# Optimization experiments

Measured on AMD Instinct MI355X. Metric: run time of the kernel, lower is better.

The kernel has to match this reference:

```python
import jax, jax.numpy as jnp
import numpy as np

ROPE_BASE = 10000.0
NUM_HEADS = 16
NUM_KV_HEADS = 4


def _rms_norm(x, eps):
    # F.rms_norm with no weight: x / sqrt(mean(x^2) + eps)
    return x * jax.lax.rsqrt(jnp.mean(x * x, axis=-1, keepdims=True) + eps)


def _apply_rope(x, cos, sin):
    h = x.shape[-1] // 2
    x1, x2 = x[..., :h], x[..., h:]
    return jnp.concatenate([x1 * cos + x2 * sin, -x1 * sin + x2 * cos], axis=-1)


def setup_inputs() -> dict:
    key = jax.random.key(0)
    ks = jax.random.split(key, 5)
    B, T, D = 2, 2048, 1024
    H, Hkv = NUM_HEADS, NUM_KV_HEADS
    hd = D // H
    kv_dim = Hkv * hd
    s_in = 1.0 / np.sqrt(D)
    return {
        "x": jax.random.normal(ks[0], (B, T, D), dtype=jnp.float32),
        "Wq": jax.random.normal(ks[1], (D, D), dtype=jnp.float32) * s_in,
        "Wk": jax.random.normal(ks[2], (kv_dim, D), dtype=jnp.float32) * s_in,
        "Wv": jax.random.normal(ks[3], (kv_dim, D), dtype=jnp.float32) * s_in,
        "Wproj": jax.random.normal(ks[4], (D, D), dtype=jnp.float32) * s_in,
        "q_gain": jnp.full((H,), 1.0, dtype=jnp.float32),
    }


def reference(x, Wq, Wk, Wv, Wproj, q_gain):
    B, T, D = x.shape
    H, Hkv = NUM_HEADS, NUM_KV_HEADS
    hd = D // H
    rep = H // Hkv
    eps = jnp.finfo(x.dtype).eps

    # QKV projections (F.linear: x @ W.T)
    q = jnp.einsum('btd,od->bto', x, Wq).reshape(B, T, H, hd).transpose(0, 2, 1, 3)
    k = jnp.einsum('btd,od->bto', x, Wk).reshape(B, T, Hkv, hd).transpose(0, 2, 1, 3)
    v = jnp.einsum('btd,od->bto', x, Wv).reshape(B, T, Hkv, hd).transpose(0, 2, 1, 3)

    q = _rms_norm(q, eps)
    k = _rms_norm(k, eps)

    # RoPE tables: [1, 1, T, hd/2]
    inv_freq = 1.0 / (ROPE_BASE ** (jnp.arange(0, hd, 2, dtype=jnp.float32) / hd))
    f = jnp.arange(T, dtype=jnp.float32)[:, None] * inv_freq[None, :]
    cos = jnp.cos(f)[None, None].astype(q.dtype)
    sin = jnp.sin(f)[None, None].astype(q.dtype)
    q = _apply_rope(q, cos, sin)
    k = _apply_rope(k, cos, sin)

    q = q * q_gain.astype(q.dtype)[None, :, None, None]

    # GQA without materializing repeated K/V: group q heads [Hkv, rep]
    qg = q.reshape(B, Hkv, rep, T, hd)
    scale = hd ** -0.5
    scores = jnp.einsum('bgrqd,bgkd->bgrqk', qg, k) * scale
    causal = jnp.tril(jnp.ones((T, T), dtype=bool))
    scores = jnp.where(causal, scores, -jnp.inf)
    att = jax.nn.softmax(scores.astype(jnp.float32), axis=-1).astype(q.dtype)
    y = jnp.einsum('bgrqk,bgkd->bgrqd', att, v)  # [B,Hkv,rep,T,hd]
    y = y.reshape(B, H, T, hd).transpose(0, 2, 1, 3).reshape(B, T, D)
    return jnp.einsum('btd,od->bto', y, Wproj)
```

## Files before the change

kernel.cpp:

```cpp
#include <hip/hip_runtime.h>
#include <cstdint>
#include <cstddef>

typedef __attribute__((ext_vector_type(8))) short short8;
typedef __attribute__((ext_vector_type(4))) float floatx4;
typedef __attribute__((ext_vector_type(4))) short short4v;
typedef unsigned short u16;
typedef unsigned int u32;

#define B_   2
#define T_   2048
#define D_   1024
#define H_   16
#define HKV_ 4
#define HD_  64
#define KV_  256
#define M_   4096
#define QS_  1536

#define NX   4194304
#define NWQ  1048576
#define NWK  262144
#define NWV  262144
#define NWP  1048576
#define NCAST (NX + NWQ + NWK + NWV + NWP)
#define CAST_BLOCKS (NCAST / 1024)
#define TAB_BLOCKS  256

__device__ __forceinline__ float b2f(u16 u) {
    union { u32 i; float f; } v; v.i = ((u32)u) << 16; return v.f;
}
__device__ __forceinline__ u16 f2b(float f) {
    union { float f; u32 i; } v; v.f = f;
    u32 r = v.i + 0x7FFF + ((v.i >> 16) & 1);
    return (u16)(r >> 16);
}
__device__ __forceinline__ u32 pack_hi(float a, float b) {
    union { float f; u32 u; } ua, ub; ua.f = a; ub.f = b;
    return (ua.u >> 16) | (ub.u & 0xFFFF0000u);
}

__device__ __forceinline__ void async16(const u16* g, u16* l) {
    __builtin_amdgcn_global_load_lds(
        (const __attribute__((address_space(1))) u32*)g,
        (__attribute__((address_space(3))) u32*)l, 16, 0, 0);
}

__global__ __launch_bounds__(256) void prep(const float* __restrict__ x,
                                            const float* __restrict__ wq,
                                            const float* __restrict__ wk,
                                            const float* __restrict__ wv,
                                            const float* __restrict__ wp,
                                            u16* __restrict__ dst,
                                            float2* __restrict__ tab) {
    int blk = blockIdx.x;
    if (blk < CAST_BLOCKS) {
        int i = blk * 1024 + threadIdx.x * 4;
        const float* src; int off;
        if      (i < NX)                  { src = x;  off = i; }
        else if (i < NX+NWQ)              { src = wq; off = i - NX; }
        else if (i < NX+NWQ+NWK)          { src = wk; off = i - (NX+NWQ); }
        else if (i < NX+NWQ+NWK+NWV)      { src = wv; off = i - (NX+NWQ+NWK); }
        else                              { src = wp; off = i - (NX+NWQ+NWK+NWV); }
        float4 v = *(const float4*)(src + off);
        short4v o;
        o.x = (short)f2b(v.x); o.y = (short)f2b(v.y);
        o.z = (short)f2b(v.z); o.w = (short)f2b(v.w);
        *(short4v*)(dst + i) = o;
    } else {
        int idx = (blk - CAST_BLOCKS) * 256 + threadIdx.x;
        int t = idx >> 5, i = idx & 31;
        float freq = exp2f(-(float)i * (13.287712379549449f / 32.0f));
        float ang = (float)t * freq;
        tab[idx] = make_float2(cosf(ang), sinf(ang));
    }
}

__global__ __launch_bounds__(256, 3) void gemm_qkv(const u16* __restrict__ A,
                                                   const u16* __restrict__ W,
                                                   u16* __restrict__ C,
                                                   u16* __restrict__ Vt,
                                                   const float* __restrict__ gain,
                                                   const float2* __restrict__ tab) {
    const int K = D_;
    __shared__ u16 As[2][128 * 32];
    __shared__ u16 Bs[2][64 * 32];
    const int t = threadIdx.x;
    const int wave = t >> 6, lane = t & 63;
    const int quad = lane >> 4, l16 = lane & 15;
    const int wm = wave * 32;
    const int m0 = blockIdx.y * 128, n0 = blockIdx.x * 64;

    floatx4 acc[2][4];
#pragma unroll
    for (int i = 0; i < 2; i++)
#pragma unroll
        for (int j = 0; j < 4; j++) acc[i][j] = (floatx4){0.f, 0.f, 0.f, 0.f};

    const int sr = t >> 2, sc = (t & 3) * 8;
    const u16* ga = A + (size_t)(m0 + sr) * K + sc;
    const u16* gb = W + (size_t)(n0 + sr) * K + sc;

    async16(ga, As[0] + t * 8);
    async16(ga + (size_t)64 * K, As[0] + t * 8 + 64 * 32);
    async16(gb, Bs[0] + t * 8);

    int cur = 0;
    for (int kt = 0; kt < K; kt += 32) {
        __syncthreads();
        if (kt + 32 < K) {
            const u16* ga2 = ga + kt + 32;
            const u16* gb2 = gb + kt + 32;
            async16(ga2, As[cur ^ 1] + t * 8);
            async16(ga2 + (size_t)64 * K, As[cur ^ 1] + t * 8 + 64 * 32);
            async16(gb2, Bs[cur ^ 1] + t * 8);
        }
        short8 af[2], bf[4];
#pragma unroll
        for (int mt = 0; mt < 2; mt++)
            af[mt] = *(const short8*)(As[cur] + (wm + mt * 16 + l16) * 32 + quad * 8);
#pragma unroll
        for (int nt = 0; nt < 4; nt++)
            bf[nt] = *(const short8*)(Bs[cur] + (nt * 16 + l16) * 32 + quad * 8);
#pragma unroll
        for (int mt = 0; mt < 2; mt++)
#pragma unroll
            for (int nt = 0; nt < 4; nt++)
                acc[mt][nt] = __builtin_amdgcn_mfma_f32_16x16x32_bf16(
                    af[mt], bf[nt], acc[mt][nt], 0, 0, 0);
        cur ^= 1;
    }

    const int col0 = n0;
    if (col0 < 1280) {
        float gs = (col0 < 1024)
                 ? gain[col0 >> 6] * (0.125f * 1.4426950408889634f)
                 : 1.0f;
#pragma unroll
        for (int mt = 0; mt < 2; mt++)
#pragma unroll
            for (int r = 0; r < 4; r++) {
                int row = m0 + wm + mt * 16 + quad * 4 + r;
                int tt = row & (T_ - 1);
                float v0 = acc[mt][0][r], v1 = acc[mt][1][r];
                float v2 = acc[mt][2][r], v3 = acc[mt][3][r];
                float ss = v0 * v0 + v1 * v1 + v2 * v2 + v3 * v3;
                ss += __shfl_xor(ss, 1); ss += __shfl_xor(ss, 2);
                ss += __shfl_xor(ss, 4); ss += __shfl_xor(ss, 8);
                float inv = rsqrtf(ss * (1.0f / 64.0f) + 1.1920929e-7f);
                v0 *= inv; v1 *= inv; v2 *= inv; v3 *= inv;
                float2 cs0 = tab[tt * 32 + l16];
                float2 cs1 = tab[tt * 32 + 16 + l16];
                float o0 = (v0 * cs0.x + v2 * cs0.y) * gs;
                float o1 = (v1 * cs1.x + v3 * cs1.y) * gs;
                float o2 = (v2 * cs0.x - v0 * cs0.y) * gs;
                float o3 = (v3 * cs1.x - v1 * cs1.y) * gs;
                u16* cp = C + (size_t)row * QS_ + col0 + l16;
                cp[0]  = f2b(o0);
                cp[16] = f2b(o1);
                cp[32] = f2b(o2);
                cp[48] = f2b(o3);
            }
    } else {
        const int g = (col0 - 1280) >> 6;
#pragma unroll
        for (int mt = 0; mt < 2; mt++)
#pragma unroll
            for (int r = 0; r < 4; r++) {
                int row = m0 + wm + mt * 16 + quad * 4 + r;
                int tt = row & (T_ - 1);
                int bb = row >> 11;
#pragma unroll
                for (int nt = 0; nt < 4; nt++)
                    Vt[(size_t)((bb * 4 + g) * 64 + nt * 16 + l16) * T_ + tt] =
                        f2b(acc[mt][nt][r]);
            }
    }
}

__global__ __launch_bounds__(256, 3) void gemm_proj(const u16* __restrict__ A,
                                                    const u16* __restrict__ W,
                                                    float* __restrict__ C) {
    const int K = D_;
    __shared__ u16 As[2][128 * 32];
    __shared__ u16 Bs[2][64 * 32];
    const int t = threadIdx.x;
    const int wave = t >> 6, lane = t & 63;
    const int quad = lane >> 4, l16 = lane & 15;
    const int wm = wave * 32;
    const int m0 = blockIdx.y * 128, n0 = blockIdx.x * 64;

    floatx4 acc[2][4];
#pragma unroll
    for (int i = 0; i < 2; i++)
#pragma unroll
        for (int j = 0; j < 4; j++) acc[i][j] = (floatx4){0.f, 0.f, 0.f, 0.f};

    const int sr = t >> 2, sc = (t & 3) * 8;
    const u16* ga = A + (size_t)(m0 + sr) * K + sc;
    const u16* gb = W + (size_t)(n0 + sr) * K + sc;

    async16(ga, As[0] + t * 8);
    async16(ga + (size_t)64 * K, As[0] + t * 8 + 64 * 32);
    async16(gb, Bs[0] + t * 8);

    int cur = 0;
    for (int kt = 0; kt < K; kt += 32) {
        __syncthreads();
        if (kt + 32 < K) {
            const u16* ga2 = ga + kt + 32;
            const u16* gb2 = gb + kt + 32;
            async16(ga2, As[cur ^ 1] + t * 8);
            async16(ga2 + (size_t)64 * K, As[cur ^ 1] + t * 8 + 64 * 32);
            async16(gb2, Bs[cur ^ 1] + t * 8);
        }
        short8 af[2], bf[4];
#pragma unroll
        for (int mt = 0; mt < 2; mt++)
            af[mt] = *(const short8*)(As[cur] + (wm + mt * 16 + l16) * 32 + quad * 8);
#pragma unroll
        for (int nt = 0; nt < 4; nt++)
            bf[nt] = *(const short8*)(Bs[cur] + (nt * 16 + l16) * 32 + quad * 8);
#pragma unroll
        for (int mt = 0; mt < 2; mt++)
#pragma unroll
            for (int nt = 0; nt < 4; nt++)
                acc[mt][nt] = __builtin_amdgcn_mfma_f32_16x16x32_bf16(
                    af[mt], bf[nt], acc[mt][nt], 0, 0, 0);
        cur ^= 1;
    }

#pragma unroll
    for (int mt = 0; mt < 2; mt++)
#pragma unroll
        for (int nt = 0; nt < 4; nt++)
#pragma unroll
            for (int r = 0; r < 4; r++) {
                int row = m0 + wm + mt * 16 + quad * 4 + r;
                int col = n0 + nt * 16 + l16;
                C[(size_t)row * D_ + col] = acc[mt][nt][r];
            }
}

__global__ __launch_bounds__(256) void flash(const u16* __restrict__ QKV,
                                             const u16* __restrict__ Vtr,
                                             u16* __restrict__ Y) {
    const int xp = blockIdx.x;
    const int h  = blockIdx.y;
    const int b  = blockIdx.z;
    const int g  = h >> 2;
    const int w    = threadIdx.x >> 6;
    const int lane = threadIdx.x & 63;
    const int quad = lane >> 4, l16 = lane & 15;

    __shared__ u16 Kt[64 * 64];
    __shared__ u16 Vs[64 * 64];
    __shared__ __align__(16) u16 P[4][2][16][72];

    const int mA = xp * 64 + w * 16;
    const int mB = (31 - xp) * 64 + w * 16;
    const int nA = xp + 1;
    const int nB = 32 - xp;

    const u16* qpA = QKV + (size_t)(b * T_ + mA + l16) * QS_ + h * HD_ + quad * 8;
    const u16* qpB = QKV + (size_t)(b * T_ + mB + l16) * QS_ + h * HD_ + quad * 8;
    short8 aqA0 = *(const short8*)(qpA);
    short8 aqA1 = *(const short8*)(qpA + 32);
    short8 aqB0 = *(const short8*)(qpB);
    short8 aqB1 = *(const short8*)(qpB + 32);

    short8 ones;
#pragma unroll
    for (int i = 0; i < 8; i++) ones[i] = (short)0x3F80;

    floatx4 accA[4], accB[4];
#pragma unroll
    for (int i = 0; i < 4; i++) {
        accA[i] = (floatx4){0.f, 0.f, 0.f, 0.f};
        accB[i] = (floatx4){0.f, 0.f, 0.f, 0.f};
    }
    floatx4 lAcc = (floatx4){0.f, 0.f, 0.f, 0.f};
    floatx4 lBcc = (floatx4){0.f, 0.f, 0.f, 0.f};

    const int srow = w * 16 + (lane >> 3);
    const int sseg = (lane & 7) ^ ((lane >> 3) & 7);
    const u16* kg = QKV + (size_t)(b * T_ + srow) * QS_ + D_ + g * 64 + sseg * 8;
    const u16* vg = Vtr + (size_t)((b * 4 + g) * 64 + srow) * T_ + sseg * 8;
    u16* klds = Kt + w * 1024 + lane * 8;
    u16* vlds = Vs + w * 1024 + lane * 8;

    const int sw0 = (quad ^ (l16 & 7)) * 8;
    const int sw1 = ((4 + quad) ^ (l16 & 7)) * 8;

    async16(kg, klds);
    async16(kg + (size_t)8 * QS_, klds + 512);
    async16(vg, vlds);
    async16(vg + (size_t)8 * T_, vlds + 512);

    for (int tk = 0; tk < nB; tk++) {
        const bool dual = (tk < nA);
        __syncthreads();

        floatx4 SB[4], SA[4];
#pragma unroll
        for (int nt = 0; nt < 4; nt++) {
            const u16* kr = Kt + (nt * 16 + l16) * 64;
            short8 kf0 = *(const short8*)(kr + sw0);
            short8 kf1 = *(const short8*)(kr + sw1);
            SB[nt] = (floatx4){0.f, 0.f, 0.f, 0.f};
            SB[nt] = __builtin_amdgcn_mfma_f32_16x16x32_bf16(kf0, aqB0, SB[nt], 0, 0, 0);
            SB[nt] = __builtin_amdgcn_mfma_f32_16x16x32_bf16(kf1, aqB1, SB[nt], 0, 0, 0);
            if (dual) {
                SA[nt] = (floatx4){0.f, 0.f, 0.f, 0.f};
                SA[nt] = __builtin_amdgcn_mfma_f32_16x16x32_bf16(kf0, aqA0, SA[nt], 0, 0, 0);
                SA[nt] = __builtin_amdgcn_mfma_f32_16x16x32_bf16(kf1, aqA1, SA[nt], 0, 0, 0);
            }
        }
        short8 vf[4][2];
#pragma unroll
        for (int dd = 0; dd < 4; dd++) {
            const u16* vr = Vs + (dd * 16 + l16) * 64;
            vf[dd][0] = *(const short8*)(vr + sw0);
            vf[dd][1] = *(const short8*)(vr + sw1);
        }
        __syncthreads();
        if (tk + 1 < nB) {
            kg += (size_t)64 * QS_;
            vg += 64;
            async16(kg, klds);
            async16(kg + (size_t)8 * QS_, klds + 512);
            async16(vg, vlds);
            async16(vg + (size_t)8 * T_, vlds + 512);
        }

        const bool maskB = (tk == nB - 1);
        const int qB = mB + l16;
#pragma unroll
        for (int nt = 0; nt < 4; nt++) {
            float p[4];
#pragma unroll
            for (int r = 0; r < 4; r++) {
                float e = __builtin_amdgcn_exp2f(SB[nt][r]);
                if (maskB) {
                    int key = tk * 64 + nt * 16 + quad * 4 + r;
                    e = (key <= qB) ? e : 0.f;
                }
                p[r] = e;
            }
            uint2 pw; pw.x = pack_hi(p[0], p[1]); pw.y = pack_hi(p[2], p[3]);
            *(uint2*)&P[w][1][l16][nt * 16 + quad * 4] = pw;
        }
        short8 pfB0 = *(const short8*)&P[w][1][l16][quad * 8];
        short8 pfB1 = *(const short8*)&P[w][1][l16][quad * 8 + 32];
#pragma unroll
        for (int dd = 0; dd < 4; dd++) {
            accB[dd] = __builtin_amdgcn_mfma_f32_16x16x32_bf16(pfB0, vf[dd][0], accB[dd], 0, 0, 0);
            accB[dd] = __builtin_amdgcn_mfma_f32_16x16x32_bf16(pfB1, vf[dd][1], accB[dd], 0, 0, 0);
        }
        lBcc = __builtin_amdgcn_mfma_f32_16x16x32_bf16(pfB0, ones, lBcc, 0, 0, 0);
        lBcc = __builtin_amdgcn_mfma_f32_16x16x32_bf16(pfB1, ones, lBcc, 0, 0, 0);

        if (dual) {
            const bool maskA = (tk == nA - 1);
            const int qA = mA + l16;
#pragma unroll
            for (int nt = 0; nt < 4; nt++) {
                float p[4];
#pragma unroll
                for (int r = 0; r < 4; r++) {
                    float e = __builtin_amdgcn_exp2f(SA[nt][r]);
                    if (maskA) {
                        int key = tk * 64 + nt * 16 + quad * 4 + r;
                        e = (key <= qA) ? e : 0.f;
                    }
                    p[r] = e;
                }
                uint2 pw; pw.x = pack_hi(p[0], p[1]); pw.y = pack_hi(p[2], p[3]);
                *(uint2*)&P[w][0][l16][nt * 16 + quad * 4] = pw;
            }
            short8 pfA0 = *(const short8*)&P[w][0][l16][quad * 8];
            short8 pfA1 = *(const short8*)&P[w][0][l16][quad * 8 + 32];
#pragma unroll
            for (int dd = 0; dd < 4; dd++) {
                accA[dd] = __builtin_amdgcn_mfma_f32_16x16x32_bf16(pfA0, vf[dd][0], accA[dd], 0, 0, 0);
                accA[dd] = __builtin_amdgcn_mfma_f32_16x16x32_bf16(pfA1, vf[dd][1], accA[dd], 0, 0, 0);
            }
            lAcc = __builtin_amdgcn_mfma_f32_16x16x32_bf16(pfA0, ones, lAcc, 0, 0, 0);
            lAcc = __builtin_amdgcn_mfma_f32_16x16x32_bf16(pfA1, ones, lAcc, 0, 0, 0);
        }
    }

#pragma unroll
    for (int r = 0; r < 4; r++) {
        float invA = 1.0f / lAcc[r];
        float invB = 1.0f / lBcc[r];
        int rowA = mA + quad * 4 + r;
        int rowB = mB + quad * 4 + r;
        u16* ypA = Y + (size_t)(b * T_ + rowA) * D_ + h * HD_ + l16;
        u16* ypB = Y + (size_t)(b * T_ + rowB) * D_ + h * HD_ + l16;
#pragma unroll
        for (int dd = 0; dd < 4; dd++) {
            ypA[dd * 16] = f2b(accA[dd][r] * invA);
            ypB[dd * 16] = f2b(accB[dd][r] * invB);
        }
    }
}

extern "C" void kernel_launch(void* const* d_in, const int* in_sizes, int n_in,
                              void* d_out, int out_size, void* d_ws, size_t ws_size,
                              hipStream_t stream) {
    const float* x    = (const float*)d_in[0];
    const float* Wq   = (const float*)d_in[1];
    const float* Wk   = (const float*)d_in[2];
    const float* Wv   = (const float*)d_in[3];
    const float* Wp   = (const float*)d_in[4];
    const float* gain = (const float*)d_in[5];
    float* out = (float*)d_out;

    u16* xb   = (u16*)d_ws;
    u16* Wcat = xb + (size_t)NX;
    u16* Wpb  = Wcat + (size_t)(NWQ + NWK + NWV);
    u16* QKV  = Wpb + (size_t)NWP;
    u16* Vt   = QKV + (size_t)M_ * QS_;
    u16* Y    = Vt + (size_t)M_ * KV_;
    float2* tab = (float2*)(Y + (size_t)M_ * D_);

    prep<<<CAST_BLOCKS + TAB_BLOCKS, 256, 0, stream>>>(x, Wq, Wk, Wv, Wp, xb, tab);

    gemm_qkv<<<dim3(QS_ / 64, M_ / 128), 256, 0, stream>>>(xb, Wcat, QKV, Vt,
                                                           gain, tab);

    flash<<<dim3(16, H_, B_), 256, 0, stream>>>(QKV, Vt, Y);

    gemm_proj<<<dim3(D_ / 64, M_ / 128), 256, 0, stream>>>(Y, Wpb, out);
}
```

Baseline: 174.1 us.

## Split flash KV range and proj GEMM K across more blocks with atomics

The flash kernel grid doubles: each original pair of query tiles is split so later query rows' key ranges are divided between two blocks. Partial unnormalized outputs and row sums for the second half of the sequence go to fp32 buffers via atomics, and a new combine kernel normalizes them into Y. The projection GEMM is split-K in two with atomicAdd into a zeroed output. The aim is more blocks and better CU occupancy, at the cost of memsets, atomic traffic, an extra kernel launch and non-deterministic summation order.

```diff
diff --git a/kernel.cpp b/kernel.cpp
--- a/kernel.cpp
+++ b/kernel.cpp
@@ -189,6 +189,7 @@
     const int quad = lane >> 4, l16 = lane & 15;
     const int wm = wave * 32;
     const int m0 = blockIdx.y * 128, n0 = blockIdx.x * 64;
+    const int kbase = blockIdx.z * 512;
 
     floatx4 acc[2][4];
 #pragma unroll
@@ -197,17 +198,17 @@
         for (int j = 0; j < 4; j++) acc[i][j] = (floatx4){0.f, 0.f, 0.f, 0.f};
 
     const int sr = t >> 2, sc = (t & 3) * 8;
-    const u16* ga = A + (size_t)(m0 + sr) * K + sc;
-    const u16* gb = W + (size_t)(n0 + sr) * K + sc;
+    const u16* ga = A + (size_t)(m0 + sr) * K + kbase + sc;
+    const u16* gb = W + (size_t)(n0 + sr) * K + kbase + sc;
 
     async16(ga, As[0] + t * 8);
     async16(ga + (size_t)64 * K, As[0] + t * 8 + 64 * 32);
     async16(gb, Bs[0] + t * 8);
 
     int cur = 0;
-    for (int kt = 0; kt < K; kt += 32) {
+    for (int kt = 0; kt < 512; kt += 32) {
         __syncthreads();
-        if (kt + 32 < K) {
+        if (kt + 32 < 512) {
             const u16* ga2 = ga + kt + 32;
             const u16* gb2 = gb + kt + 32;
             async16(ga2, As[cur ^ 1] + t * 8);
@@ -238,14 +239,16 @@
             for (int r = 0; r < 4; r++) {
                 int row = m0 + wm + mt * 16 + quad * 4 + r;
                 int col = n0 + nt * 16 + l16;
-                C[(size_t)row * D_ + col] = acc[mt][nt][r];
-            }
-}
-
-__global__ __launch_bounds__(256) void flash(const u16* __restrict__ QKV,
-                                             const u16* __restrict__ Vtr,
-                                             u16* __restrict__ Y) {
-    const int xp = blockIdx.x;
+                atomicAdd(&C[(size_t)row * D_ + col], acc[mt][nt][r]);
+            }
+}
+
+__global__ __launch_bounds__(256, 4) void flash(const u16* __restrict__ QKV,
+                                                const u16* __restrict__ Vtr,
+                                                u16* __restrict__ Y,
+                                                float* __restrict__ Oacc,
+                                                float* __restrict__ Lacc) {
+    const int u  = blockIdx.x;
     const int h  = blockIdx.y;
     const int b  = blockIdx.z;
     const int g  = h >> 2;
@@ -255,155 +258,148 @@
 
     __shared__ u16 Kt[64 * 64];
     __shared__ u16 Vs[64 * 64];
-    __shared__ __align__(16) u16 P[4][2][16][72];
-
-    const int mA = xp * 64 + w * 16;
-    const int mB = (31 - xp) * 64 + w * 16;
-    const int nA = xp + 1;
-    const int nB = 32 - xp;
-
-    const u16* qpA = QKV + (size_t)(b * T_ + mA + l16) * QS_ + h * HD_ + quad * 8;
-    const u16* qpB = QKV + (size_t)(b * T_ + mB + l16) * QS_ + h * HD_ + quad * 8;
-    short8 aqA0 = *(const short8*)(qpA);
-    short8 aqA1 = *(const short8*)(qpA + 32);
-    short8 aqB0 = *(const short8*)(qpB);
-    short8 aqB1 = *(const short8*)(qpB + 32);
-
-    short8 ones;
-#pragma unroll
-    for (int i = 0; i < 8; i++) ones[i] = (short)0x3F80;
-
-    floatx4 accA[4], accB[4];
-#pragma unroll
-    for (int i = 0; i < 4; i++) {
-        accA[i] = (floatx4){0.f, 0.f, 0.f, 0.f};
-        accB[i] = (floatx4){0.f, 0.f, 0.f, 0.f};
-    }
-    floatx4 lAcc = (floatx4){0.f, 0.f, 0.f, 0.f};
-    floatx4 lBcc = (floatx4){0.f, 0.f, 0.f, 0.f};
+    __shared__ __align__(16) u16 P[4][16][72];
+
+    const int xp = u & 15;
+    const int nseg = (u < 16) ? 2 : 1;
+    int m0s[2], k0s[2], k1s[2];
+    if (u < 16) {
+        m0s[0] = xp * 64;        k0s[0] = 0;  k1s[0] = xp + 1;
+        m0s[1] = (31 - xp) * 64; k0s[1] = 16; k1s[1] = 32 - xp;
+    } else {
+        m0s[0] = (31 - xp) * 64; k0s[0] = 0;  k1s[0] = 16;
+        m0s[1] = 0; k0s[1] = 0; k1s[1] = 0;
+    }
 
     const int srow = w * 16 + (lane >> 3);
     const int sseg = (lane & 7) ^ ((lane >> 3) & 7);
-    const u16* kg = QKV + (size_t)(b * T_ + srow) * QS_ + D_ + g * 64 + sseg * 8;
-    const u16* vg = Vtr + (size_t)((b * 4 + g) * 64 + srow) * T_ + sseg * 8;
+    const u16* kgb = QKV + (size_t)(b * T_ + srow) * QS_ + D_ + g * 64 + sseg * 8;
+    const u16* vgb = Vtr + (size_t)((b * 4 + g) * 64 + srow) * T_ + sseg * 8;
     u16* klds = Kt + w * 1024 + lane * 8;
     u16* vlds = Vs + w * 1024 + lane * 8;
-
     const int sw0 = (quad ^ (l16 & 7)) * 8;
     const int sw1 = ((4 + quad) ^ (l16 & 7)) * 8;
 
-    async16(kg, klds);
-    async16(kg + (size_t)8 * QS_, klds + 512);
-    async16(vg, vlds);
-    async16(vg + (size_t)8 * T_, vlds + 512);
-
-    for (int tk = 0; tk < nB; tk++) {
-        const bool dual = (tk < nA);
-        __syncthreads();
-
-        floatx4 SB[4], SA[4];
-#pragma unroll
-        for (int nt = 0; nt < 4; nt++) {
-            const u16* kr = Kt + (nt * 16 + l16) * 64;
-            short8 kf0 = *(const short8*)(kr + sw0);
-            short8 kf1 = *(const short8*)(kr + sw1);
-            SB[nt] = (floatx4){0.f, 0.f, 0.f, 0.f};
-            SB[nt] = __builtin_amdgcn_mfma_f32_16x16x32_bf16(kf0, aqB0, SB[nt], 0, 0, 0);
-            SB[nt] = __builtin_amdgcn_mfma_f32_16x16x32_bf16(kf1, aqB1, SB[nt], 0, 0, 0);
-            if (dual) {
-                SA[nt] = (floatx4){0.f, 0.f, 0.f, 0.f};
-                SA[nt] = __builtin_amdgcn_mfma_f32_16x16x32_bf16(kf0, aqA0, SA[nt], 0, 0, 0);
-                SA[nt] = __builtin_amdgcn_mfma_f32_16x16x32_bf16(kf1, aqA1, SA[nt], 0, 0, 0);
-            }
-        }
-        short8 vf[4][2];
-#pragma unroll
-        for (int dd = 0; dd < 4; dd++) {
-            const u16* vr = Vs + (dd * 16 + l16) * 64;
-            vf[dd][0] = *(const short8*)(vr + sw0);
-            vf[dd][1] = *(const short8*)(vr + sw1);
-        }
-        __syncthreads();
-        if (tk + 1 < nB) {
-            kg += (size_t)64 * QS_;
-            vg += 64;
-            async16(kg, klds);
-            async16(kg + (size_t)8 * QS_, klds + 512);
-            async16(vg, vlds);
-            async16(vg + (size_t)8 * T_, vlds + 512);
-        }
-
-        const bool maskB = (tk == nB - 1);
-        const int qB = mB + l16;
-#pragma unroll
-        for (int nt = 0; nt < 4; nt++) {
-            float p[4];
-#pragma unroll
-            for (int r = 0; r < 4; r++) {
-                float e = __builtin_amdgcn_exp2f(SB[nt][r]);
-                if (maskB) {
-                    int key = tk * 64 + nt * 16 + quad * 4 + r;
-                    e = (key <= qB) ? e : 0.f;
-                }
-                p[r] = e;
-            }
-            uint2 pw; pw.x = pack_hi(p[0], p[1]); pw.y = pack_hi(p[2], p[3]);
-            *(uint2*)&P[w][1][l16][nt * 16 + quad * 4] = pw;
-        }
-        short8 pfB0 = *(const short8*)&P[w][1][l16][quad * 8];
-        short8 pfB1 = *(const short8*)&P[w][1][l16][quad * 8 + 32];
-#pragma unroll
-        for (int dd = 0; dd < 4; dd++) {
-            accB[dd] = __builtin_amdgcn_mfma_f32_16x16x32_bf16(pfB0, vf[dd][0], accB[dd], 0, 0, 0);
-            accB[dd] = __builtin_amdgcn_mfma_f32_16x16x32_bf16(pfB1, vf[dd][1], accB[dd], 0, 0, 0);
-        }
-        lBcc = __builtin_amdgcn_mfma_f32_16x16x32_bf16(pfB0, ones, lBcc, 0, 0, 0);
-        lBcc = __builtin_amdgcn_mfma_f32_16x16x32_bf16(pfB1, ones, lBcc, 0, 0, 0);
-
-        if (dual) {
-            const bool maskA = (tk == nA - 1);
-            const int qA = mA + l16;
+    auto stage = [&](int tile) {
+        const u16* kg = kgb + (size_t)tile * 64 * QS_;
+        const u16* vg = vgb + (size_t)tile * 64;
+        async16(kg, klds);
+        async16(kg + (size_t)8 * QS_, klds + 512);
+        async16(vg, vlds);
+        async16(vg + (size_t)8 * T_, vlds + 512);
+    };
+
+    short8 ones;
+#pragma unroll
+    for (int i = 0; i < 8; i++) ones[i] = (short)0x3F80;
+
+    stage(k0s[0]);
+
+    for (int seg = 0; seg < nseg; ++seg) {
+        const int mseg = m0s[seg], k0 = k0s[seg], k1 = k1s[seg];
+        const int jt = mseg >> 6;
+        const int m = mseg + w * 16;
+
+        const u16* qp = QKV + (size_t)(b * T_ + m + l16) * QS_ + h * HD_ + quad * 8;
+        short8 aq0 = *(const short8*)(qp);
+        short8 aq1 = *(const short8*)(qp + 32);
+
+        floatx4 acc[4];
+#pragma unroll
+        for (int i = 0; i < 4; i++) acc[i] = (floatx4){0.f, 0.f, 0.f, 0.f};
+        floatx4 lAcc = (floatx4){0.f, 0.f, 0.f, 0.f};
+
+        for (int tk = k0; tk < k1; ++tk) {
+            __syncthreads();
+
+            floatx4 S[4];
+#pragma unroll
+            for (int nt = 0; nt < 4; nt++) {
+                const u16* kr = Kt + (nt * 16 + l16) * 64;
+                short8 kf0 = *(const short8*)(kr + sw0);
+                short8 kf1 = *(const short8*)(kr + sw1);
+                S[nt] = (floatx4){0.f, 0.f, 0.f, 0.f};
+                S[nt] = __builtin_amdgcn_mfma_f32_16x16x32_bf16(kf0, aq0, S[nt], 0, 0, 0);
+                S[nt] = __builtin_amdgcn_mfma_f32_16x16x32_bf16(kf1, aq1, S[nt], 0, 0, 0);
+            }
+            short8 vf[4][2];
+#pragma unroll
+            for (int dd = 0; dd < 4; dd++) {
+                const u16* vr = Vs + (dd * 16 + l16) * 64;
+                vf[dd][0] = *(const short8*)(vr + sw0);
+                vf[dd][1] = *(const short8*)(vr + sw1);
+            }
+            __syncthreads();
+
+            int nxt = (tk + 1 < k1) ? tk + 1 : ((seg + 1 < nseg) ? k0s[seg + 1] : -1);
+            if (nxt >= 0) stage(nxt);
+
+            const bool msk = (tk == jt);
+            const int qq = m + l16;
 #pragma unroll
             for (int nt = 0; nt < 4; nt++) {
                 float p[4];
 #pragma unroll
                 for (int r = 0; r < 4; r++) {
-                    float e = __builtin_amdgcn_exp2f(SA[nt][r]);
-                    if (maskA) {
+                    float e = __builtin_amdgcn_exp2f(S[nt][r]);
+                    if (msk) {
                         int key = tk * 64 + nt * 16 + quad * 4 + r;
-                        e = (key <= qA) ? e : 0.f;
+                        e = (key <= qq) ? e : 0.f;
                     }
                     p[r] = e;
                 }
                 uint2 pw; pw.x = pack_hi(p[0], p[1]); pw.y = pack_hi(p[2], p[3]);
-                *(uint2*)&P[w][0][l16][nt * 16 + quad * 4] = pw;
-            }
-            short8 pfA0 = *(const short8*)&P[w][0][l16][quad * 8];
-            short8 pfA1 = *(const short8*)&P[w][0][l16][quad * 8 + 32];
+                *(uint2*)&P[w][l16][nt * 16 + quad * 4] = pw;
+            }
+            short8 pf0 = *(const short8*)&P[w][l16][quad * 8];
+            short8 pf1 = *(const short8*)&P[w][l16][quad * 8 + 32];
 #pragma unroll
             for (int dd = 0; dd < 4; dd++) {
-                accA[dd] = __builtin_amdgcn_mfma_f32_16x16x32_bf16(pfA0, vf[dd][0], accA[dd], 0, 0, 0);
-                accA[dd] = __builtin_amdgcn_mfma_f32_16x16x32_bf16(pfA1, vf[dd][1], accA[dd], 0, 0, 0);
-            }
-            lAcc = __builtin_amdgcn_mfma_f32_16x16x32_bf16(pfA0, ones, lAcc, 0, 0, 0);
-            lAcc = __builtin_amdgcn_mfma_f32_16x16x32_bf16(pfA1, ones, lAcc, 0, 0, 0);
+                acc[dd] = __builtin_amdgcn_mfma_f32_16x16x32_bf16(pf0, vf[dd][0], acc[dd], 0, 0, 0);
+                acc[dd] = __builtin_amdgcn_mfma_f32_16x16x32_bf16(pf1, vf[dd][1], acc[dd], 0, 0, 0);
+            }
+            lAcc = __builtin_amdgcn_mfma_f32_16x16x32_bf16(pf0, ones, lAcc, 0, 0, 0);
+            lAcc = __builtin_amdgcn_mfma_f32_16x16x32_bf16(pf1, ones, lAcc, 0, 0, 0);
         }
-    }
-
-#pragma unroll
-    for (int r = 0; r < 4; r++) {
-        float invA = 1.0f / lAcc[r];
-        float invB = 1.0f / lBcc[r];
-        int rowA = mA + quad * 4 + r;
-        int rowB = mB + quad * 4 + r;
-        u16* ypA = Y + (size_t)(b * T_ + rowA) * D_ + h * HD_ + l16;
-        u16* ypB = Y + (size_t)(b * T_ + rowB) * D_ + h * HD_ + l16;
-#pragma unroll
-        for (int dd = 0; dd < 4; dd++) {
-            ypA[dd * 16] = f2b(accA[dd][r] * invA);
-            ypB[dd * 16] = f2b(accB[dd][r] * invB);
+
+        if (u < 16 && seg == 0) {
+#pragma unroll
+            for (int r = 0; r < 4; r++) {
+                float inv = 1.0f / lAcc[r];
+                int row = m + quad * 4 + r;
+                u16* yp = Y + (size_t)(b * T_ + row) * D_ + h * HD_ + l16;
+#pragma unroll
+                for (int dd = 0; dd < 4; dd++)
+                    yp[dd * 16] = f2b(acc[dd][r] * inv);
+            }
+        } else {
+#pragma unroll
+            for (int r = 0; r < 4; r++) {
+                int rp = m + quad * 4 + r - 1024;
+                float* op = Oacc + (size_t)(b * 1024 + rp) * 1024 + h * HD_ + l16;
+#pragma unroll
+                for (int dd = 0; dd < 4; dd++)
+                    atomicAdd(op + dd * 16, acc[dd][r]);
+                if (l16 == 0)
+                    atomicAdd(Lacc + (b * 1024 + rp) * 16 + h, lAcc[r]);
+            }
         }
     }
+}
+
+__global__ __launch_bounds__(256) void combine(const float* __restrict__ Oacc,
+                                               const float* __restrict__ Lacc,
+                                               u16* __restrict__ Y) {
+    int e = (blockIdx.x * 256 + threadIdx.x) * 4;
+    int b = e >> 20;
+    int rem = e & 1048575;
+    int row = rem >> 10, col = rem & 1023;
+    float inv = 1.0f / Lacc[(b * 1024 + row) * 16 + (col >> 6)];
+    float4 o = *(const float4*)(Oacc + (size_t)(b * 1024 + row) * 1024 + col);
+    short4v y;
+    y.x = (short)f2b(o.x * inv); y.y = (short)f2b(o.y * inv);
+    y.z = (short)f2b(o.z * inv); y.w = (short)f2b(o.w * inv);
+    *(short4v*)(Y + (size_t)(b * T_ + 1024 + row) * D_ + col) = y;
 }
 
 extern "C" void kernel_launch(void* const* d_in, const int* in_sizes, int n_in,
@@ -424,13 +420,21 @@
     u16* Vt   = QKV + (size_t)M_ * QS_;
     u16* Y    = Vt + (size_t)M_ * KV_;
     float2* tab = (float2*)(Y + (size_t)M_ * D_);
+    float* Oacc = (float*)(tab + 65536);
+    float* Lacc = Oacc + (size_t)2 * 1024 * 1024;
+
+    hipMemsetAsync(out, 0, (size_t)M_ * D_ * 4, stream);
+    hipMemsetAsync(Oacc, 0, (size_t)2 * 1024 * 1024 * 4, stream);
+    hipMemsetAsync(Lacc, 0, (size_t)2 * 1024 * 16 * 4, stream);
 
     prep<<<CAST_BLOCKS + TAB_BLOCKS, 256, 0, stream>>>(x, Wq, Wk, Wv, Wp, xb, tab);
 
     gemm_qkv<<<dim3(QS_ / 64, M_ / 128), 256, 0, stream>>>(xb, Wcat, QKV, Vt,
                                                            gain, tab);
 
-    flash<<<dim3(16, H_, B_), 256, 0, stream>>>(QKV, Vt, Y);
-
-    gemm_proj<<<dim3(D_ / 64, M_ / 128), 256, 0, stream>>>(Y, Wpb, out);
-}
+    flash<<<dim3(32, H_, B_), 256, 0, stream>>>(QKV, Vt, Y, Oacc, Lacc);
+
+    combine<<<2048, 256, 0, stream>>>(Oacc, Lacc, Y);
+
+    gemm_proj<<<dim3(D_ / 64, M_ / 128, 2), 256, 0, stream>>>(Y, Wpb, out);
+}
```

After: 195.9 us. 12.6% more time.
